# Kernel tuning notes

Hardware: AMD Instinct MI355X
Metric: run time of the kernel (lower is better)

Reference implementation:

```python
import jax, jax.numpy as jnp
import numpy as np

DIM, HEADS = 1024, 16
HEAD_DIM = DIM // HEADS
SCALE = HEAD_DIM ** -0.5


def setup_inputs() -> dict:
    key = jax.random.key(0)
    ks = jax.random.split(key, 5)
    B, N = 2, 2048
    x = jax.random.normal(ks[0], (B, N, DIM), dtype=jnp.float32)
    freqs = jax.random.normal(ks[1], (N, HEAD_DIM // 2), dtype=jnp.float32)
    w_qkv = jax.random.normal(ks[2], (3 * DIM, DIM), dtype=jnp.float32) * 0.02
    w_proj = jax.random.normal(ks[3], (DIM, DIM), dtype=jnp.float32) * 0.02
    b_proj = jnp.zeros((DIM,), dtype=jnp.float32)
    return {"x": x, "freqs": freqs, "w_qkv": w_qkv, "w_proj": w_proj, "b_proj": b_proj}


def _apply_rotary(t, cos, sin):
    # t: (B,N,H,D); cos/sin: (1,N,1,D//2)
    B, N, H, D = t.shape
    tp = t.reshape(B, N, H, D // 2, 2)
    x1, x2 = tp[..., 0], tp[..., 1]
    out = jnp.stack([x1 * cos - x2 * sin, x1 * sin + x2 * cos], axis=-1)
    return out.reshape(B, N, H, D)


def reference(x, freqs, w_qkv, w_proj, b_proj):
    B, N, C = x.shape
    H, D = HEADS, HEAD_DIM
    qkv = (x @ w_qkv.T).reshape(B, N, 3, H, D)  # fused QKV projection
    q, k, v = qkv[:, :, 0], qkv[:, :, 1], qkv[:, :, 2]  # each (B,N,H,D)
    cos = jnp.cos(freqs)[None, :, None, :]  # (1,N,1,D/2)
    sin = jnp.sin(freqs)[None, :, None, :]
    q = _apply_rotary(q, cos, sin)
    k = _apply_rotary(k, cos, sin)
    # SDPA: scores (B,H,N,N)
    scores = jnp.einsum("bqhd,bkhd->bhqk", q, k) * SCALE
    attn = jax.nn.softmax(scores, axis=-1)
    out = jnp.einsum("bhqk,bkhd->bqhd", attn, v).reshape(B, N, C)
    return out @ w_proj.T + b_proj
```

## Files before the change

kernel.cpp:

```cpp
#include <hip/hip_runtime.h>
#include <hip/hip_bf16.h>
#include <stdint.h>

#define BATCH   2
#define SEQ     2048
#define CDIM    1024
#define NHEAD   16
#define HDIM    64
#define MROWS   (BATCH*SEQ)
#define QKVN    (3*CDIM)
#define QSCALE  0.18033688011112042f

typedef __hip_bfloat16 bf16;
using bf16x8 = __attribute__((ext_vector_type(8))) __bf16;
using f32x4  = __attribute__((ext_vector_type(4))) float;
using s16x4  = __attribute__((ext_vector_type(4))) short;

__device__ __forceinline__ void gld16(const void* g, void* l) {
    __builtin_amdgcn_global_load_lds(
        (__attribute__((address_space(1))) void*)(void*)(g),
        (__attribute__((address_space(3))) void*)(l),
        16, 0, 0);
}

__device__ __forceinline__ f32x4 mfma16x16x32(bf16x8 a, bf16x8 b, f32x4 c) {
    return __builtin_amdgcn_mfma_f32_16x16x32_bf16(a, b, c, 0, 0, 0);
}
__device__ __forceinline__ f32x4 mfma16x16x16(s16x4 a, s16x4 b, f32x4 c) {
    return __builtin_amdgcn_mfma_f32_16x16x16bf16_1k(a, b, c, 0, 0, 0);
}

__device__ __forceinline__ uint16_t bfbits(float v) {
    bf16 b = __float2bfloat16(v);
    return *(uint16_t*)&b;
}
__device__ __forceinline__ uint32_t pkbf(float a, float b) {
    uint32_t au = __builtin_bit_cast(uint32_t, a);
    uint32_t bu = __builtin_bit_cast(uint32_t, b);
    return ((au + 0x8000u) >> 16) | ((bu + 0x8000u) & 0xffff0000u);
}
__device__ __forceinline__ void store_out(bf16* p, float v) { *p = __float2bfloat16(v); }
__device__ __forceinline__ void store_out(float* p, float v) { *p = v; }

#define NX_F4 ((size_t)MROWS*CDIM/4)
#define NQ_F4 ((size_t)QKVN*CDIM/4)
#define NP_F4 ((size_t)CDIM*CDIM/4)
#define NF_SC ((size_t)SEQ*32)

__global__ __launch_bounds__(256)
void cvt_kernel(const float* __restrict__ x, const float* __restrict__ wq,
                const float* __restrict__ wp, const float* __restrict__ freqs,
                bf16* __restrict__ xb, bf16* __restrict__ wqb,
                bf16* __restrict__ wpb, float2* __restrict__ csn) {
    size_t i4 = (size_t)blockIdx.x*256 + threadIdx.x;
    if (i4 < NX_F4 + NQ_F4 + NP_F4) {
        const float* src; bf16* dst; size_t off;
        if (i4 < NX_F4)           { src = x;  dst = xb;  off = i4; }
        else if (i4 < NX_F4+NQ_F4){ src = wq; dst = wqb; off = i4 - NX_F4; }
        else                      { src = wp; dst = wpb; off = i4 - NX_F4 - NQ_F4; }
        float4 v = ((const float4*)src)[off];
        bf16 o[4] = { __float2bfloat16(v.x), __float2bfloat16(v.y),
                      __float2bfloat16(v.z), __float2bfloat16(v.w) };
        *(uint64_t*)(dst + off*4) = *(const uint64_t*)o;
    } else if (i4 < NX_F4 + NQ_F4 + NP_F4 + NF_SC) {
        size_t k = i4 - (NX_F4 + NQ_F4 + NP_F4);
        float f = freqs[k];
        csn[k] = make_float2(cosf(f), sinf(f));
    }
}

__global__ __launch_bounds__(256)
void gemm_qkv_rope(const bf16* __restrict__ A, const bf16* __restrict__ Bw,
                   const float2* __restrict__ csn, bf16* __restrict__ Qr,
                   bf16* __restrict__ Kr, bf16* __restrict__ VG) {
    const int K = CDIM;
    __shared__ __align__(16) bf16 sh[64*136];
    bf16* As = sh;
    bf16* Bs = sh + 4096;

    const int bm = blockIdx.x, bn = blockIdx.y;
    const int tid  = threadIdx.x;
    const int lane = tid & 63;
    const int w    = tid >> 6;
    const int wm   = (w & 1) * 64;
    const int wn   = (w >> 1) * 64;
    const int quad = lane >> 4;
    const int l16  = lane & 15;

    const int c0 = tid, c1 = tid + 256;
    const size_t a_off0 = (size_t)(bm*128 + (c0 >> 2)) * K + (c0 & 3) * 8;
    const size_t a_off1 = (size_t)(bm*128 + (c1 >> 2)) * K + (c1 & 3) * 8;
    const size_t b_off0 = (size_t)(bn*128 + (c0 >> 2)) * K + (c0 & 3) * 8;
    const size_t b_off1 = (size_t)(bn*128 + (c1 >> 2)) * K + (c1 & 3) * 8;

    f32x4 acc[4][4] = {};

    for (int k0 = 0; k0 < K; k0 += 32) {
        __syncthreads();
        gld16(A + a_off0 + k0, &As[c0*8]);
        gld16(A + a_off1 + k0, &As[c1*8]);
        gld16(Bw + b_off0 + k0, &Bs[c0*8]);
        gld16(Bw + b_off1 + k0, &Bs[c1*8]);
        __syncthreads();

        bf16x8 af[4], bfv[4];
#pragma unroll
        for (int i = 0; i < 4; i++)
            af[i] = *(const bf16x8*)&As[(wm + i*16 + l16)*32 + quad*8];
#pragma unroll
        for (int i = 0; i < 4; i++)
            bfv[i] = *(const bf16x8*)&Bs[(wn + i*16 + l16)*32 + quad*8];
#pragma unroll
        for (int mi = 0; mi < 4; mi++)
#pragma unroll
            for (int ni = 0; ni < 4; ni++)
                acc[mi][ni] = mfma16x16x32(af[mi], bfv[ni], acc[mi][ni]);
    }

    const int region = bn >> 3;
    if (region < 2) {
        bf16* dst = region ? Kr : Qr;
        const float qs = region ? 1.0f : QSCALE;
        const int odd = l16 & 1;
#pragma unroll
        for (int mi = 0; mi < 4; mi++) {
#pragma unroll
            for (int ni = 0; ni < 4; ni++) {
                const int cq = (bn & 7)*128 + wn + ni*16 + l16;
                const int h = cq >> 6, d = cq & 63, fi = d >> 1;
#pragma unroll
                for (int r = 0; r < 4; r++) {
                    const int m = bm*128 + wm + mi*16 + quad*4 + r;
                    const int bb = m >> 11, n = m & 2047;
                    float own = acc[mi][ni][r];
                    float prt = __shfl_xor(own, 1);
                    float2 cs2 = csn[n*32 + fi];
                    float o = odd ? (prt*cs2.y + own*cs2.x)
                                  : (own*cs2.x - prt*cs2.y);
                    dst[((size_t)(bb*16 + h)*SEQ + n)*HDIM + d] =
                        __float2bfloat16(o * qs);
                }
            }
        }
    } else {
        const int bb = (bm*128) >> 11, n0l = (bm*128) & 2047;
        __syncthreads();
#pragma unroll
        for (int cc = 0; cc < 2; ++cc) {
            if ((w >> 1) == cc) {
#pragma unroll
                for (int mi = 0; mi < 4; mi++)
#pragma unroll
                    for (int ni = 0; ni < 4; ni++) {
                        const int d  = ni*16 + l16;
                        const int tl = wm + mi*16 + quad*4;
                        uint2 pk;
                        pk.x = (uint32_t)bfbits(acc[mi][ni][0]) |
                               ((uint32_t)bfbits(acc[mi][ni][1]) << 16);
                        pk.y = (uint32_t)bfbits(acc[mi][ni][2]) |
                               ((uint32_t)bfbits(acc[mi][ni][3]) << 16);
                        *(uint2*)&sh[d*136 + tl] = pk;
                    }
            }
            __syncthreads();
            const int h = (bn - 16)*2 + cc;
            bf16* vg = VG + (size_t)(bb*16 + h) * (SEQ*HDIM);
#pragma unroll
            for (int k = 0; k < 8; k++) {
                int s8   = tid + 256*k;
                int tile = s8 >> 10, si = s8 & 1023;
                int g  = si >> 6,  ln = si & 63;
                int j  = g >> 2,   dt = g & 3;
                int qk = ln >> 4,  ld = ln & 15;
                int tl = tile*64 + j*16 + qk*4;
                int d  = dt*16 + ld;
                *(uint2*)&vg[(size_t)((n0l >> 6) + tile)*4096 + si*4] =
                    *(const uint2*)&sh[d*136 + tl];
            }
            __syncthreads();
        }
    }
}

template<typename OutT, bool ADD_BIAS>
__global__ __launch_bounds__(256)
void gemm_bt(const bf16* __restrict__ A, const bf16* __restrict__ Bw,
             const float* __restrict__ bias, OutT* __restrict__ C,
             int M, int N, int K) {
    __shared__ __align__(16) bf16 As[128*32];
    __shared__ __align__(16) bf16 Bs[128*32];

    const int bm = blockIdx.x, bn = blockIdx.y;
    const int tid  = threadIdx.x;
    const int lane = tid & 63;
    const int w    = tid >> 6;
    const int wm   = (w & 1) * 64;
    const int wn   = (w >> 1) * 64;
    const int quad = lane >> 4;
    const int l16  = lane & 15;

    const int c0 = tid, c1 = tid + 256;
    const size_t a_off0 = (size_t)(bm*128 + (c0 >> 2)) * K + (c0 & 3) * 8;
    const size_t a_off1 = (size_t)(bm*128 + (c1 >> 2)) * K + (c1 & 3) * 8;
    const size_t b_off0 = (size_t)(bn*128 + (c0 >> 2)) * K + (c0 & 3) * 8;
    const size_t b_off1 = (size_t)(bn*128 + (c1 >> 2)) * K + (c1 & 3) * 8;

    f32x4 acc[4][4] = {};

    for (int k0 = 0; k0 < K; k0 += 32) {
        __syncthreads();
        gld16(A + a_off0 + k0, &As[c0*8]);
        gld16(A + a_off1 + k0, &As[c1*8]);
        gld16(Bw + b_off0 + k0, &Bs[c0*8]);
        gld16(Bw + b_off1 + k0, &Bs[c1*8]);
        __syncthreads();

        bf16x8 af[4], bfv[4];
#pragma unroll
        for (int i = 0; i < 4; i++)
            af[i] = *(const bf16x8*)&As[(wm + i*16 + l16)*32 + quad*8];
#pragma unroll
        for (int i = 0; i < 4; i++)
            bfv[i] = *(const bf16x8*)&Bs[(wn + i*16 + l16)*32 + quad*8];
#pragma unroll
        for (int mi = 0; mi < 4; mi++)
#pragma unroll
            for (int ni = 0; ni < 4; ni++)
                acc[mi][ni] = mfma16x16x32(af[mi], bfv[ni], acc[mi][ni]);
    }

#pragma unroll
    for (int mi = 0; mi < 4; mi++) {
        const int r0 = bm*128 + wm + mi*16 + quad*4;
#pragma unroll
        for (int ni = 0; ni < 4; ni++) {
            const int c = bn*128 + wn + ni*16 + l16;
            float bv = 0.f;
            if (ADD_BIAS) bv = bias[c];
#pragma unroll
            for (int r = 0; r < 4; r++)
                store_out(&C[(size_t)(r0 + r)*N + c], acc[mi][ni][r] + bv);
        }
    }
}

__global__ __launch_bounds__(256)
void attn_kernel(const bf16* __restrict__ Qr, const bf16* __restrict__ Kr,
                 const bf16* __restrict__ VG, bf16* __restrict__ Ao) {
    const int blk = blockIdx.x;
    const int bh  = blk >> 4;
    const int b   = bh >> 4, h = bh & 15;
    const int q0  = (blk & 15) * 128;
    const int tid = threadIdx.x;
    const int w   = tid >> 6, lane = tid & 63;
    const int quad = lane >> 4, l16 = lane & 15;

    __shared__ __align__(16) bf16 Ks[2][64*64];
    __shared__ __align__(16) bf16 Vs[2][64*64];

    bf16x8 qf[2][2];
#pragma unroll
    for (int t = 0; t < 2; t++) {
        const int qrow = q0 + w*32 + t*16 + l16;
        const bf16* qp = Qr + ((size_t)bh*SEQ + qrow)*HDIM + quad*8;
        qf[t][0] = *(const bf16x8*)(qp);
        qf[t][1] = *(const bf16x8*)(qp + 32);
    }

    const int s0 = tid, s1 = tid + 256;
    const int r0 = s0 >> 3, g0 = (s0 & 7) ^ (r0 & 7);
    const int r1 = s1 >> 3, g1 = (s1 & 7) ^ (r1 & 7);
    const bf16* kb0 = Kr + (size_t)bh*SEQ*HDIM + r0*HDIM + g0*8;
    const bf16* kb1 = Kr + (size_t)bh*SEQ*HDIM + r1*HDIM + g1*8;
    const bf16* vgb = VG + (size_t)bh*SEQ*HDIM;
    const bf16* vb0 = vgb + s0*8;
    const bf16* vb1 = vgb + s1*8;

    f32x4 acc[2][4] = {};
    float lsum[2] = {0.f, 0.f};

    gld16(kb0, &Ks[0][s0*8]);
    gld16(kb1, &Ks[0][s1*8]);
    gld16(vb0, &Vs[0][s0*8]);
    gld16(vb1, &Vs[0][s1*8]);

    const int swz = l16 & 7;

    for (int it = 0; it < SEQ/64; ++it) {
        const int cur = it & 1, nxt = cur ^ 1;
        __syncthreads();
        if (it + 1 < SEQ/64) {
            const size_t o = (size_t)(it + 1) * 4096;
            gld16(kb0 + o, &Ks[nxt][s0*8]);
            gld16(kb1 + o, &Ks[nxt][s1*8]);
            gld16(vb0 + o, &Vs[nxt][s0*8]);
            gld16(vb1 + o, &Vs[nxt][s1*8]);
        }

        f32x4 sv[2][4];
#pragma unroll
        for (int j = 0; j < 4; j++) {
            const bf16* krow = &Ks[cur][(j*16 + l16)*64];
            bf16x8 ka = *(const bf16x8*)(krow + ((quad     ^ swz) * 8));
            bf16x8 kb = *(const bf16x8*)(krow + (((quad+4) ^ swz) * 8));
#pragma unroll
            for (int t = 0; t < 2; t++) {
                f32x4 tacc = {};
                tacc = mfma16x16x32(ka, qf[t][0], tacc);
                tacc = mfma16x16x32(kb, qf[t][1], tacc);
                sv[t][j] = tacc;
            }
        }

        s16x4 pf[2][4];
#pragma unroll
        for (int t = 0; t < 2; t++) {
#pragma unroll
            for (int j = 0; j < 4; j++) {
                float e0 = __builtin_amdgcn_exp2f(sv[t][j][0]);
                float e1 = __builtin_amdgcn_exp2f(sv[t][j][1]);
                float e2 = __builtin_amdgcn_exp2f(sv[t][j][2]);
                float e3 = __builtin_amdgcn_exp2f(sv[t][j][3]);
                lsum[t] += (e0 + e1) + (e2 + e3);
                union { uint32_t u[2]; s16x4 v; } pa;
                pa.u[0] = pkbf(e0, e1);
                pa.u[1] = pkbf(e2, e3);
                pf[t][j] = pa.v;
            }
        }

#pragma unroll
        for (int dt = 0; dt < 4; dt++) {
#pragma unroll
            for (int j = 0; j < 4; j++) {
                s16x4 vf = *(const s16x4*)&Vs[cur][((j*4 + dt)*64 + lane)*4];
                acc[0][dt] = mfma16x16x16(pf[0][j], vf, acc[0][dt]);
                acc[1][dt] = mfma16x16x16(pf[1][j], vf, acc[1][dt]);
            }
        }
    }

#pragma unroll
    for (int t = 0; t < 2; t++) {
        lsum[t] += __shfl_xor(lsum[t], 16, 64);
        lsum[t] += __shfl_xor(lsum[t], 32, 64);
    }
    float lt[2][4];
#pragma unroll
    for (int t = 0; t < 2; t++)
#pragma unroll
        for (int r = 0; r < 4; r++)
            lt[t][r] = __shfl(lsum[t], quad*20 + r, 64);

#pragma unroll
    for (int t = 0; t < 2; t++)
#pragma unroll
        for (int dt = 0; dt < 4; dt++)
#pragma unroll
            for (int r = 0; r < 4; r++) {
                int qr  = q0 + w*32 + t*16 + quad*4 + r;
                int col = h*HDIM + dt*16 + l16;
                Ao[(size_t)(b*SEQ + qr)*CDIM + col] =
                    __float2bfloat16(acc[t][dt][r] / lt[t][r]);
            }
}

extern "C" void kernel_launch(void* const* d_in, const int* in_sizes, int n_in,
                              void* d_out, int out_size, void* d_ws, size_t ws_size,
                              hipStream_t stream) {
    const float* x      = (const float*)d_in[0];
    const float* freqs  = (const float*)d_in[1];
    const float* w_qkv  = (const float*)d_in[2];
    const float* w_proj = (const float*)d_in[3];
    const float* b_proj = (const float*)d_in[4];
    float* out = (float*)d_out;

    char* ws = (char*)d_ws;
    bf16*   xb    = (bf16*)ws;   ws += (size_t)MROWS * CDIM * sizeof(bf16);
    bf16*   wqkvb = (bf16*)ws;   ws += (size_t)QKVN * CDIM * sizeof(bf16);
    bf16*   wprojb= (bf16*)ws;   ws += (size_t)CDIM * CDIM * sizeof(bf16);
    float2* csn   = (float2*)ws; ws += (size_t)SEQ * 32 * sizeof(float2);
    bf16*   Qr    = (bf16*)ws;   ws += (size_t)BATCH*NHEAD*SEQ*HDIM*sizeof(bf16);
    bf16*   Kr    = (bf16*)ws;   ws += (size_t)BATCH*NHEAD*SEQ*HDIM*sizeof(bf16);
    bf16*   VG    = (bf16*)ws;   ws += (size_t)BATCH*NHEAD*SEQ*HDIM*sizeof(bf16);
    bf16*   Ao    = (bf16*)ws;

    dim3 blk(256);
    {
        size_t nthr = NX_F4 + NQ_F4 + NP_F4 + NF_SC;
        cvt_kernel<<<dim3((nthr + 255) / 256), blk, 0, stream>>>(
            x, w_qkv, w_proj, freqs, xb, wqkvb, wprojb, csn);
    }
    gemm_qkv_rope<<<dim3(MROWS/128, QKVN/128), blk, 0, stream>>>(
        xb, wqkvb, csn, Qr, Kr, VG);
    attn_kernel<<<dim3(BATCH*NHEAD*(SEQ/128)), blk, 0, stream>>>(
        Qr, Kr, VG, Ao);
    gemm_bt<float, true><<<dim3(MROWS/128, CDIM/128), blk, 0, stream>>>(
        Ao, wprojb, b_proj, out, MROWS, CDIM, CDIM);
}
```

Measured before the change: 212.6 us.

## Restructure attention kernel to single-wave blocks with register-staged K/V fragments

The attention kernel now launches one 64-thread wave per block. Each wave handles 64 query rows across four 16-row tiles, and the block-wide __syncthreads is removed. K and V fragments are read from LDS into registers at the start of each iteration, before the next tile's global-to-LDS prefetch is issued, so the double buffer no longer needs a barrier. This costs twice as much K/V traffic per query row, lower occupancy per CU under the same 32KB LDS footprint, and reliance on the compiler to place the waits for the asynchronous LDS loads.

```diff
diff --git a/kernel.cpp b/kernel.cpp
--- a/kernel.cpp
+++ b/kernel.cpp
@@ -244,83 +244,83 @@
     }
 }
 
-__global__ __launch_bounds__(256)
+__global__ __launch_bounds__(64)
 void attn_kernel(const bf16* __restrict__ Qr, const bf16* __restrict__ Kr,
                  const bf16* __restrict__ VG, bf16* __restrict__ Ao) {
     const int blk = blockIdx.x;
-    const int bh  = blk >> 4;
+    const int bh  = blk >> 5;
     const int b   = bh >> 4, h = bh & 15;
-    const int q0  = (blk & 15) * 128;
-    const int tid = threadIdx.x;
-    const int w   = tid >> 6, lane = tid & 63;
+    const int q0  = (blk & 31) * 64;
+    const int lane = threadIdx.x;
     const int quad = lane >> 4, l16 = lane & 15;
+    const int swz  = l16 & 7;
 
     __shared__ __align__(16) bf16 Ks[2][64*64];
     __shared__ __align__(16) bf16 Vs[2][64*64];
 
-    bf16x8 qf[2][2];
-#pragma unroll
-    for (int t = 0; t < 2; t++) {
-        const int qrow = q0 + w*32 + t*16 + l16;
+    bf16x8 qf[4][2];
+#pragma unroll
+    for (int t = 0; t < 4; t++) {
+        const int qrow = q0 + t*16 + l16;
         const bf16* qp = Qr + ((size_t)bh*SEQ + qrow)*HDIM + quad*8;
         qf[t][0] = *(const bf16x8*)(qp);
         qf[t][1] = *(const bf16x8*)(qp + 32);
     }
 
-    const int s0 = tid, s1 = tid + 256;
-    const int r0 = s0 >> 3, g0 = (s0 & 7) ^ (r0 & 7);
-    const int r1 = s1 >> 3, g1 = (s1 & 7) ^ (r1 & 7);
-    const bf16* kb0 = Kr + (size_t)bh*SEQ*HDIM + r0*HDIM + g0*8;
-    const bf16* kb1 = Kr + (size_t)bh*SEQ*HDIM + r1*HDIM + g1*8;
-    const bf16* vgb = VG + (size_t)bh*SEQ*HDIM;
-    const bf16* vb0 = vgb + s0*8;
-    const bf16* vb1 = vgb + s1*8;
-
-    f32x4 acc[2][4] = {};
-    float lsum[2] = {0.f, 0.f};
-
-    gld16(kb0, &Ks[0][s0*8]);
-    gld16(kb1, &Ks[0][s1*8]);
-    gld16(vb0, &Vs[0][s0*8]);
-    gld16(vb1, &Vs[0][s1*8]);
-
-    const int swz = l16 & 7;
+    const bf16* KrB = Kr + (size_t)bh*SEQ*HDIM;
+    const bf16* VgB = VG + (size_t)bh*SEQ*HDIM;
+    int koff[8];
+#pragma unroll
+    for (int k = 0; k < 8; k++) {
+        int c = lane + 64*k;
+        int r = c >> 3, g = (c & 7) ^ (r & 7);
+        koff[k] = r*HDIM + g*8;
+    }
+
+    f32x4 acc[4][4] = {};
+    float lsum[4] = {};
+
+#pragma unroll
+    for (int k = 0; k < 8; k++) {
+        gld16(KrB + koff[k], &Ks[0][(lane + 64*k)*8]);
+        gld16(VgB + (lane + 64*k)*8, &Vs[0][(lane + 64*k)*8]);
+    }
 
     for (int it = 0; it < SEQ/64; ++it) {
         const int cur = it & 1, nxt = cur ^ 1;
-        __syncthreads();
+        bf16x8 kfr[4][2];
+#pragma unroll
+        for (int j = 0; j < 4; j++) {
+            const bf16* krow = &Ks[cur][(j*16 + l16)*64];
+            kfr[j][0] = *(const bf16x8*)(krow + ((quad     ^ swz) * 8));
+            kfr[j][1] = *(const bf16x8*)(krow + (((quad+4) ^ swz) * 8));
+        }
+        s16x4 vfr[16];
+#pragma unroll
+        for (int m = 0; m < 16; m++)
+            vfr[m] = *(const s16x4*)&Vs[cur][(m*64 + lane)*4];
+
         if (it + 1 < SEQ/64) {
             const size_t o = (size_t)(it + 1) * 4096;
-            gld16(kb0 + o, &Ks[nxt][s0*8]);
-            gld16(kb1 + o, &Ks[nxt][s1*8]);
-            gld16(vb0 + o, &Vs[nxt][s0*8]);
-            gld16(vb1 + o, &Vs[nxt][s1*8]);
-        }
-
-        f32x4 sv[2][4];
+#pragma unroll
+            for (int k = 0; k < 8; k++) {
+                gld16(KrB + koff[k] + o, &Ks[nxt][(lane + 64*k)*8]);
+                gld16(VgB + (lane + 64*k)*8 + o, &Vs[nxt][(lane + 64*k)*8]);
+            }
+        }
+
+        s16x4 pf[4][4];
 #pragma unroll
         for (int j = 0; j < 4; j++) {
-            const bf16* krow = &Ks[cur][(j*16 + l16)*64];
-            bf16x8 ka = *(const bf16x8*)(krow + ((quad     ^ swz) * 8));
-            bf16x8 kb = *(const bf16x8*)(krow + (((quad+4) ^ swz) * 8));
-#pragma unroll
-            for (int t = 0; t < 2; t++) {
-                f32x4 tacc = {};
-                tacc = mfma16x16x32(ka, qf[t][0], tacc);
-                tacc = mfma16x16x32(kb, qf[t][1], tacc);
-                sv[t][j] = tacc;
-            }
-        }
-
-        s16x4 pf[2][4];
-#pragma unroll
-        for (int t = 0; t < 2; t++) {
-#pragma unroll
-            for (int j = 0; j < 4; j++) {
-                float e0 = __builtin_amdgcn_exp2f(sv[t][j][0]);
-                float e1 = __builtin_amdgcn_exp2f(sv[t][j][1]);
-                float e2 = __builtin_amdgcn_exp2f(sv[t][j][2]);
-                float e3 = __builtin_amdgcn_exp2f(sv[t][j][3]);
+#pragma unroll
+            for (int t = 0; t < 4; t++) {
+                f32x4 sv = {};
+                sv = mfma16x16x32(kfr[j][0], qf[t][0], sv);
+                sv = mfma16x16x32(kfr[j][1], qf[t][1], sv);
+                float e0 = __builtin_amdgcn_exp2f(sv[0]);
+                float e1 = __builtin_amdgcn_exp2f(sv[1]);
+                float e2 = __builtin_amdgcn_exp2f(sv[2]);
+                float e3 = __builtin_amdgcn_exp2f(sv[3]);
                 lsum[t] += (e0 + e1) + (e2 + e3);
                 union { uint32_t u[2]; s16x4 v; } pa;
                 pa.u[0] = pkbf(e0, e1);
@@ -333,32 +333,33 @@
         for (int dt = 0; dt < 4; dt++) {
 #pragma unroll
             for (int j = 0; j < 4; j++) {
-                s16x4 vf = *(const s16x4*)&Vs[cur][((j*4 + dt)*64 + lane)*4];
-                acc[0][dt] = mfma16x16x16(pf[0][j], vf, acc[0][dt]);
-                acc[1][dt] = mfma16x16x16(pf[1][j], vf, acc[1][dt]);
-            }
-        }
-    }
-
-#pragma unroll
-    for (int t = 0; t < 2; t++) {
+                s16x4 vf = vfr[j*4 + dt];
+#pragma unroll
+                for (int t = 0; t < 4; t++)
+                    acc[t][dt] = mfma16x16x16(pf[t][j], vf, acc[t][dt]);
+            }
+        }
+    }
+
+#pragma unroll
+    for (int t = 0; t < 4; t++) {
         lsum[t] += __shfl_xor(lsum[t], 16, 64);
         lsum[t] += __shfl_xor(lsum[t], 32, 64);
     }
-    float lt[2][4];
-#pragma unroll
-    for (int t = 0; t < 2; t++)
+    float lt[4][4];
+#pragma unroll
+    for (int t = 0; t < 4; t++)
 #pragma unroll
         for (int r = 0; r < 4; r++)
             lt[t][r] = __shfl(lsum[t], quad*20 + r, 64);
 
 #pragma unroll
-    for (int t = 0; t < 2; t++)
+    for (int t = 0; t < 4; t++)
 #pragma unroll
         for (int dt = 0; dt < 4; dt++)
 #pragma unroll
             for (int r = 0; r < 4; r++) {
-                int qr  = q0 + w*32 + t*16 + quad*4 + r;
+                int qr  = q0 + t*16 + quad*4 + r;
                 int col = h*HDIM + dt*16 + l16;
                 Ao[(size_t)(b*SEQ + qr)*CDIM + col] =
                     __float2bfloat16(acc[t][dt][r] / lt[t][r]);
@@ -385,16 +386,15 @@
     bf16*   VG    = (bf16*)ws;   ws += (size_t)BATCH*NHEAD*SEQ*HDIM*sizeof(bf16);
     bf16*   Ao    = (bf16*)ws;
 
-    dim3 blk(256);
     {
         size_t nthr = NX_F4 + NQ_F4 + NP_F4 + NF_SC;
-        cvt_kernel<<<dim3((nthr + 255) / 256), blk, 0, stream>>>(
+        cvt_kernel<<<dim3((nthr + 255) / 256), dim3(256), 0, stream>>>(
             x, w_qkv, w_proj, freqs, xb, wqkvb, wprojb, csn);
     }
-    gemm_qkv_rope<<<dim3(MROWS/128, QKVN/128), blk, 0, stream>>>(
+    gemm_qkv_rope<<<dim3(MROWS/128, QKVN/128), dim3(256), 0, stream>>>(
         xb, wqkvb, csn, Qr, Kr, VG);
-    attn_kernel<<<dim3(BATCH*NHEAD*(SEQ/128)), blk, 0, stream>>>(
+    attn_kernel<<<dim3(BATCH*NHEAD*(SEQ/64)), dim3(64), 0, stream>>>(
         Qr, Kr, VG, Ao);
-    gemm_bt<float, true><<<dim3(MROWS/128, CDIM/128), blk, 0, stream>>>(
+    gemm_bt<float, true><<<dim3(MROWS/128, CDIM/128), dim3(256), 0, stream>>>(
         Ao, wprojb, b_proj, out, MROWS, CDIM, CDIM);
 }
```

New measurement: 211.2 us. About the same (-0.7%).
